# Performance work log

Hardware: AMD Instinct MI355X
Metric: run time of the kernel (lower is better)

The kernel has to match this reference:

```python
import jax, jax.numpy as jnp
import numpy as np

IMSIZE = 128; R = 2; B = 2; C = 3; D = 64; Q = 128; M = 8; ITERS = 32
N = IMSIZE * IMSIZE
EPS = 1e-8


def _build_edges(S, r):
    # local (2r+1)^2 pixel neighborhood, as in build_perception(imsize, perception_size)
    ys, xs = np.meshgrid(np.arange(S), np.arange(S), indexing='ij')
    rows, cols = [], []
    for dy in range(-r, r + 1):
        for dx in range(-r, r + 1):
            ny, nx = ys + dy, xs + dx
            ok = (ny >= 0) & (ny < S) & (nx >= 0) & (nx < S)
            rows.append((ys * S + xs)[ok])
            cols.append((ny * S + nx)[ok])
    return (np.concatenate(rows).astype(np.int32), np.concatenate(cols).astype(np.int32))


def _conv(x, w, b=None):
    y = jax.lax.conv_general_dilated(x, w, (1, 1), 'SAME', dimension_numbers=('NHWC', 'HWIO', 'NHWC'))
    return y if b is None else y + b


def _bn(x, g, b):
    mu = x.mean((0, 1, 2))
    var = x.var((0, 1, 2))
    return (x - mu) * jax.lax.rsqrt(var + 1e-5) * g + b


def _resblock(f, w1, g1, t1, w2, g2, t2):
    h = jax.nn.relu(_bn(_conv(f, w1), g1, t1))
    h = _bn(_conv(h, w2), g2, t2)
    return jax.nn.relu(f + h)


def _forward(x, w_bb1, b_bb1, w_bb2, b_bb2,
             w_k1, g_k1, t_k1, w_k2, g_k2, t_k2, w_kp, b_kp,
             w_q1, g_q1, t_q1, w_q2, g_q2, t_q2, w_qp,
             h0, row, col, agent_idx):
    # conv backbone (preserves spatial resolution)
    f = jax.nn.relu(_conv(x, w_bb1, b_bb1))
    f = jax.nn.relu(_conv(f, w_bb2, b_bb2))
    # key / query heads: ResidualBlock + 1x1 conv
    ks = _conv(_resblock(f, w_k1, g_k1, t_k1, w_k2, g_k2, t_k2), w_kp, b_kp).reshape(B, N, D)
    qs = _conv(_resblock(f, w_q1, g_q1, t_q1, w_q2, g_q2, t_q2), w_qp).reshape(B, N, D)
    # edge-gather cosine similarity (torch.cosine_similarity with eps=1e-8)
    qe = qs[:, row]          # [B, E, D]
    ke = ks[:, col]          # [B, E, D]
    weights = (qe * ke).sum(-1) / (
        jnp.maximum(jnp.linalg.norm(qe, axis=-1), EPS) *
        jnp.maximum(jnp.linalg.norm(ke, axis=-1), EPS))   # [B, E]

    # 32-iteration sparse adjacency propagation: h <- normalize(A @ h)
    def step(h, _):
        msg = jnp.zeros_like(h).at[:, row, :].add(weights[:, :, None] * h[:, col, :])
        h = msg / jnp.maximum(jnp.linalg.norm(msg, axis=-1, keepdims=True), EPS)
        return h, None

    h, _ = jax.lax.scan(step, h0, None, length=ITERS)     # [B, N, Q]

    # competition routing: pixels compete for M agent slots via cosine affinity
    pix = h / jnp.maximum(jnp.linalg.norm(h, axis=-1, keepdims=True), EPS)
    ag = pix[:, agent_idx]                                # [B, M, Q]
    sim = jnp.einsum('bnq,bmq->bnm', pix, ag)
    masks = jax.nn.softmax(sim * 10.0, axis=-1)           # [B, N, M]
    return masks.reshape(B, IMSIZE, IMSIZE, M).transpose(0, 3, 1, 2)  # [B, M, W, H]


def setup_inputs() -> dict:
    key = jax.random.key(0)
    k = jax.random.split(key, 12)
    s = 0.05
    row, col = _build_edges(IMSIZE, R)
    agent_idx = np.linspace(0, N - 1, M).astype(np.int32)
    return dict(
        x=jax.random.normal(k[0], (B, IMSIZE, IMSIZE, C), jnp.float32),
        w_bb1=jax.random.normal(k[1], (3, 3, C, D), jnp.float32) * s, b_bb1=jnp.zeros((D,), jnp.float32),
        w_bb2=jax.random.normal(k[2], (3, 3, D, D), jnp.float32) * s, b_bb2=jnp.zeros((D,), jnp.float32),
        w_k1=jax.random.normal(k[3], (3, 3, D, D), jnp.float32) * s,
        g_k1=jnp.ones((D,), jnp.float32), t_k1=jnp.zeros((D,), jnp.float32),
        w_k2=jax.random.normal(k[4], (3, 3, D, D), jnp.float32) * s,
        g_k2=jnp.ones((D,), jnp.float32), t_k2=jnp.zeros((D,), jnp.float32),
        w_kp=jax.random.normal(k[5], (1, 1, D, D), jnp.float32) * s, b_kp=jnp.zeros((D,), jnp.float32),
        w_q1=jax.random.normal(k[6], (3, 3, D, D), jnp.float32) * s,
        g_q1=jnp.ones((D,), jnp.float32), t_q1=jnp.zeros((D,), jnp.float32),
        w_q2=jax.random.normal(k[7], (3, 3, D, D), jnp.float32) * s,
        g_q2=jnp.ones((D,), jnp.float32), t_q2=jnp.zeros((D,), jnp.float32),
        w_qp=jax.random.normal(k[8], (1, 1, D, D), jnp.float32) * s,
        h0=jax.random.normal(k[9], (B, N, Q), jnp.float32),
        row=jnp.asarray(row), col=jnp.asarray(col),
        agent_idx=jnp.asarray(agent_idx),
    )


def reference(x, w_bb1, b_bb1, w_bb2, b_bb2,
              w_k1, g_k1, t_k1, w_k2, g_k2, t_k2, w_kp, b_kp,
              w_q1, g_q1, t_q1, w_q2, g_q2, t_q2, w_qp,
              h0, row, col, agent_idx):
    return _forward(x, w_bb1, b_bb1, w_bb2, b_bb2,
                    w_k1, g_k1, t_k1, w_k2, g_k2, t_k2, w_kp, b_kp,
                    w_q1, g_q1, t_q1, w_q2, g_q2, t_q2, w_qp,
                    h0, row, col, agent_idx)
```

## Files before the change

### kernel.cpp

```cpp
#include <hip/hip_runtime.h>
#include <math.h>

#define NPIX 16384
#define EPSF 1e-8f

typedef float f32x4 __attribute__((ext_vector_type(4)));
typedef short s16x8 __attribute__((ext_vector_type(8)));

__device__ __forceinline__ float wred64(float s){
  s += __shfl_xor(s, 32); s += __shfl_xor(s, 16); s += __shfl_xor(s, 8);
  s += __shfl_xor(s, 4);  s += __shfl_xor(s, 2);  s += __shfl_xor(s, 1);
  return s;
}
__device__ __forceinline__ float rdlane(float v, int l){
  return __int_as_float(__builtin_amdgcn_readlane(__float_as_int(v), l));
}
__device__ __forceinline__ float dot4f(float4 a, float4 b, float acc){
  acc = fmaf(a.x,b.x,acc); acc = fmaf(a.y,b.y,acc);
  acc = fmaf(a.z,b.z,acc); acc = fmaf(a.w,b.w,acc);
  return acc;
}
__device__ __forceinline__ void bf16split(float v, unsigned short &hi, unsigned short &lo){
  unsigned u = __float_as_uint(v);
  unsigned r = u + 0x7FFFu + ((u >> 16) & 1u);
  hi = (unsigned short)(r >> 16);
  float hf = __uint_as_float(((unsigned)hi) << 16);
  float l = v - hf;
  unsigned u2 = __float_as_uint(l);
  unsigned r2 = u2 + 0x7FFFu + ((u2 >> 16) & 1u);
  lo = (unsigned short)(r2 >> 16);
}

__global__ __launch_bounds__(256) void prep_kernel(const float* __restrict__ w_bb2, const float* __restrict__ w_k1,
                            const float* __restrict__ w_k2, const float* __restrict__ w_q1,
                            const float* __restrict__ w_q2, const float* __restrict__ w_kp,
                            const float* __restrict__ w_qp, unsigned short* __restrict__ wh,
                            unsigned short* __restrict__ wl, float* __restrict__ wtp,
                            float* __restrict__ stats){
  int gid = blockIdx.x*256 + threadIdx.x;
  if (gid < 184320){
    int j = gid & 7;
    int t1 = gid >> 3;
    int lane = t1 & 63;
    int t2 = t1 >> 6;
    int kb = t2 % 18;
    int t3 = t2 / 18;
    int ct = t3 & 3;
    int c  = t3 >> 2;
    const float* src = c==0? w_bb2 : c==1? w_k1 : c==2? w_k2 : c==3? w_q1 : w_q2;
    int cout = ct*16 + (lane & 15);
    int k = kb*32 + (lane>>4)*8 + j;
    float v = src[k*64 + cout];
    unsigned short h,l; bf16split(v,h,l);
    wh[gid] = h; wl[gid] = l;
  } else if (gid < 192512){
    int t = gid - 184320; int which = t >> 12; int d = t & 4095;
    const float* src = which ? w_qp : w_kp;
    int k = d & 3, cout = (d>>2) & 63, cin4 = d >> 8;
    wtp[t] = src[(cin4*4 + k)*64 + cout];
  } else if (gid < 193024){
    stats[gid - 192512] = 0.f;
  }
}

__global__ __launch_bounds__(256) void conv1_kernel(const float* __restrict__ x, const float* __restrict__ w,
                                                    const float* __restrict__ bias, float* __restrict__ out){
  int wv = blockIdx.x*4 + (threadIdx.x >> 6);
  int c  = threadIdx.x & 63;
  int p0 = wv << 3;
  int ub = __builtin_amdgcn_readfirstlane(p0);
  int b  = ub >> 14; int i0 = ub & (NPIX-1);
  int y  = i0 >> 7, x0 = i0 & 127;
  float wv_[9][3];
  #pragma unroll
  for (int t=0;t<9;++t)
    #pragma unroll
    for (int ci=0;ci<3;++ci) wv_[t][ci] = w[(t*3+ci)*64 + c];
  float bv = bias[c];
  float acc[8];
  #pragma unroll
  for (int p=0;p<8;++p) acc[p] = bv;
  for (int ky=0; ky<3; ++ky){
    int ny = y + ky - 1;
    if ((unsigned)ny >= 128u) continue;
    const float* rowp = x + ((b<<14) + ny*128)*3;
    for (int kx=0; kx<3; ++kx){
      int t = ky*3 + kx;
      #pragma unroll
      for (int p=0;p<8;++p){
        int col = x0 + p + kx - 1;
        if ((unsigned)col < 128u){
          const float* ip = rowp + col*3;
          acc[p] = fmaf(ip[0], wv_[t][0], acc[p]);
          acc[p] = fmaf(ip[1], wv_[t][1], acc[p]);
          acc[p] = fmaf(ip[2], wv_[t][2], acc[p]);
        }
      }
    }
  }
  float* op = out + (p0 << 6) + c;
  #pragma unroll
  for (int p=0;p<8;++p) op[p*64] = fmaxf(acc[p], 0.f);
}

__global__ __launch_bounds__(512) void conv3m_kernel(const float* __restrict__ in,
    const unsigned short* __restrict__ wh, const unsigned short* __restrict__ wl,
    const float* __restrict__ bias, int relu,
    const float* __restrict__ bnst, const float* __restrict__ bng, const float* __restrict__ bnb,
    float* __restrict__ out, float* __restrict__ ost){
  __shared__ unsigned short lhi[12672];
  __shared__ unsigned short llo[12672];
  __shared__ float lout[4352];
  __shared__ float la[64], lb[64];
  __shared__ float ls1[64], ls2[64];
  int blk = blockIdx.x;
  int xh = blk & 1, y = (blk>>1) & 127, b = blk >> 8;
  int x0 = xh << 6;
  int tid = threadIdx.x;
  if (tid < 64){
    float a = 1.f, bo = 0.f;
    if (bnst){
      float mu  = bnst[tid] * (1.f/32768.f);
      float var = bnst[64+tid] * (1.f/32768.f) - mu*mu;
      a  = bng[tid] * rsqrtf(var + 1e-5f);
      bo = bnb[tid] - mu*a;
    }
    la[tid] = a; lb[tid] = bo;
    ls1[tid] = 0.f; ls2[tid] = 0.f;
  }
  __syncthreads();
  for (int s = tid; s < 3168; s += 512){
    int pr = s >> 4, cq = s & 15;
    int ky = pr / 66, px = pr - ky*66;
    int ny = y + ky - 1, gx = x0 - 1 + px;
    float v0=0.f, v1=0.f, v2=0.f, v3=0.f;
    if ((unsigned)ny < 128u && (unsigned)gx < 128u){
      const float* ip = in + (((b<<14) + ny*128 + gx)<<6) + (cq<<2);
      float4 t = *(const float4*)ip;
      int c0 = cq<<2;
      v0 = fmaxf(fmaf(t.x, la[c0],   lb[c0]),   0.f);
      v1 = fmaxf(fmaf(t.y, la[c0+1], lb[c0+1]), 0.f);
      v2 = fmaxf(fmaf(t.z, la[c0+2], lb[c0+2]), 0.f);
      v3 = fmaxf(fmaf(t.w, la[c0+3], lb[c0+3]), 0.f);
    }
    unsigned short h0,l0,h1,l1,h2,l2,h3,l3;
    bf16split(v0,h0,l0); bf16split(v1,h1,l1); bf16split(v2,h2,l2); bf16split(v3,h3,l3);
    int slot = (cq >> 1) ^ (pr & 7);
    int byte = pr*128 + (slot<<4) + ((cq & 1) << 3);
    *(uint2*)((char*)lhi + byte) = make_uint2((unsigned)h0 | ((unsigned)h1<<16),
                                              (unsigned)h2 | ((unsigned)h3<<16));
    *(uint2*)((char*)llo + byte) = make_uint2((unsigned)l0 | ((unsigned)l1<<16),
                                              (unsigned)l2 | ((unsigned)l3<<16));
  }
  __syncthreads();
  int lane = tid & 63, wid = tid >> 6;
  int pxsub = wid & 3, ch = wid >> 2;
  int col16 = lane & 15, kgrp = lane >> 4;
  f32x4 acc0 = {0.f,0.f,0.f,0.f}, acc1 = acc0, acl0 = acc0, acl1 = acc0;
  int abase = (ch*2*18)*512 + lane*8;
  #pragma unroll
  for (int kb=0; kb<18; ++kb){
    int tap = kb >> 1;
    int ky = (tap >= 6) ? 2 : (tap >= 3 ? 1 : 0);
    int kx = tap - ky*3;
    int pr = ky*66 + pxsub*16 + col16 + kx;
    int ci0 = ((kb & 1) << 5) + (kgrp << 3);
    int byte = pr*128 + ((((ci0 >> 3) ^ (pr & 7))) << 4);
    s16x8 Bh = *(const s16x8*)((const char*)lhi + byte);
    s16x8 Bl = *(const s16x8*)((const char*)llo + byte);
    int ao = abase + kb*512;
    s16x8 Ah0 = *(const s16x8*)(wh + ao);
    s16x8 Al0 = *(const s16x8*)(wl + ao);
    s16x8 Ah1 = *(const s16x8*)(wh + ao + 9216);
    s16x8 Al1 = *(const s16x8*)(wl + ao + 9216);
    acc0 = __builtin_amdgcn_mfma_f32_16x16x32_bf16(Ah0, Bh, acc0, 0, 0, 0);
    acl0 = __builtin_amdgcn_mfma_f32_16x16x32_bf16(Ah0, Bl, acl0, 0, 0, 0);
    acc1 = __builtin_amdgcn_mfma_f32_16x16x32_bf16(Ah1, Bh, acc1, 0, 0, 0);
    acl1 = __builtin_amdgcn_mfma_f32_16x16x32_bf16(Ah1, Bl, acl1, 0, 0, 0);
    acl0 = __builtin_amdgcn_mfma_f32_16x16x32_bf16(Al0, Bh, acl0, 0, 0, 0);
    acl1 = __builtin_amdgcn_mfma_f32_16x16x32_bf16(Al1, Bh, acl1, 0, 0, 0);
  }
  acc0 = acc0 + acl0;
  acc1 = acc1 + acl1;
  int pxl = pxsub*16 + col16;
  int co0 = ch*32 + kgrp*4;
  *(f32x4*)(lout + pxl*68 + co0)      = acc0;
  *(f32x4*)(lout + pxl*68 + co0 + 16) = acc1;
  __syncthreads();
  {
    int px = tid >> 3, c8 = (tid & 7) << 3;
    const float* lp = lout + px*68 + c8;
    float r0[8];
    #pragma unroll
    for (int j=0;j<8;++j) r0[j] = lp[j];
    if (bias){
      #pragma unroll
      for (int j=0;j<8;++j) r0[j] += bias[c8+j];
    }
    if (relu){
      #pragma unroll
      for (int j=0;j<8;++j) r0[j] = fmaxf(r0[j], 0.f);
    }
    float* op = out + (((b<<14) + y*128 + x0 + px)<<6) + c8;
    #pragma unroll
    for (int j=0;j<8;++j) op[j] = r0[j];
    if (ost){
      float s1v[8], s2v[8];
      #pragma unroll
      for (int j=0;j<8;++j){ s1v[j] = r0[j]; s2v[j] = r0[j]*r0[j]; }
      #pragma unroll
      for (int m=8; m<64; m<<=1){
        #pragma unroll
        for (int j=0;j<8;++j){ s1v[j] += __shfl_xor(s1v[j], m); s2v[j] += __shfl_xor(s2v[j], m); }
      }
      int lane2 = tid & 63;
      if ((lane2 >> 3) == 0){
        int c0 = (lane2 & 7) << 3;
        #pragma unroll
        for (int j=0;j<8;++j){ atomicAdd(&ls1[c0+j], s1v[j]); atomicAdd(&ls2[c0+j], s2v[j]); }
      }
      __syncthreads();
      if (tid < 64){ atomicAdd(&ost[tid], ls1[tid]); atomicAdd(&ost[64+tid], ls2[tid]); }
    }
  }
}

__global__ __launch_bounds__(256) void resfuse_kernel(float* __restrict__ t, const float* __restrict__ f,
                                                      const float* __restrict__ stats, const float* __restrict__ g,
                                                      const float* __restrict__ beta){
  int idx4 = blockIdx.x*256 + threadIdx.x;
  float4 v = ((float4*)t)[idx4];
  float4 fv = ((const float4*)f)[idx4];
  int c0 = (idx4 & 15) * 4;
  float a[4], bb[4];
  #pragma unroll
  for (int j=0;j<4;++j){
    int c = c0 + j;
    float mu  = stats[c]    * (1.f/32768.f);
    float var = stats[64+c] * (1.f/32768.f) - mu*mu;
    a[j]  = g[c] * rsqrtf(var + 1e-5f);
    bb[j] = beta[c] - mu*a[j];
  }
  v.x = fmaxf(fv.x + fmaf(v.x, a[0], bb[0]), 0.f);
  v.y = fmaxf(fv.y + fmaf(v.y, a[1], bb[1]), 0.f);
  v.z = fmaxf(fv.z + fmaf(v.z, a[2], bb[2]), 0.f);
  v.w = fmaxf(fv.w + fmaf(v.w, a[3], bb[3]), 0.f);
  ((float4*)t)[idx4] = v;
}

__global__ __launch_bounds__(256) void proj_kernel(const float* __restrict__ r, const float* __restrict__ wt1,
                                                   const float* __restrict__ bias, float* __restrict__ out,
                                                   float* __restrict__ nrm){
  int wv = blockIdx.x*4 + (threadIdx.x >> 6);
  int c  = threadIdx.x & 63;
  int p0 = wv << 3;
  int ub = __builtin_amdgcn_readfirstlane(p0);
  const float4* wq = (const float4*)wt1 + c;
  float4 w[16];
  #pragma unroll
  for (int q=0;q<16;++q) w[q] = wq[q*64];
  float bv = bias ? bias[c] : 0.f;
  #pragma unroll
  for (int p=0;p<8;++p){
    const float* ip = r + ((ub + p) << 6);
    float a0 = bv, a1 = 0.f;
    #pragma unroll
    for (int q=0;q<16;q+=2){
      float4 i0 = *(const float4*)(ip + (q<<2));
      float4 i1 = *(const float4*)(ip + ((q+1)<<2));
      a0 = dot4f(i0, w[q],   a0);
      a1 = dot4f(i1, w[q+1], a1);
    }
    float acc = a0 + a1;
    out[((p0+p)<<6) + c] = acc;
    float s = wred64(acc*acc);
    if (c == 0) nrm[p0+p] = sqrtf(s);
  }
}

#define EW_PAD 68
__global__ __launch_bounds__(256) void edge_kernel(const float* __restrict__ qs, const float* __restrict__ ks,
                                                   const float* __restrict__ nq, const float* __restrict__ nk,
                                                   float* __restrict__ W){
  __shared__ float klds[100*EW_PAD];
  __shared__ float qlds[16*EW_PAD];
  int blk = blockIdx.x;
  int b = blk >> 10; int rem = blk & 1023;
  int y = rem >> 3; int x0 = (rem & 7) << 4;
  int tid = threadIdx.x;
  for (int s = tid; s < 1600; s += 256){
    int cin4 = s & 15; int col = (s >> 4) % 20; int r = (s >> 4) / 20;
    int ry = y - 2 + r; ry = ry < 0 ? 0 : (ry > 127 ? 127 : ry);
    int cx = x0 - 2 + col; cx = cx < 0 ? 0 : (cx > 127 ? 127 : cx);
    float4 v = *(const float4*)(ks + (((b<<14) + ry*128 + cx)<<6) + cin4*4);
    *(float4*)(klds + (r*20+col)*EW_PAD + cin4*4) = v;
  }
  {
    int cin4 = tid & 15; int px = tid >> 4;
    float4 v = *(const float4*)(qs + (((b<<14) + y*128 + x0 + px)<<6) + cin4*4);
    *(float4*)(qlds + px*EW_PAD + cin4*4) = v;
  }
  __syncthreads();
  #pragma unroll
  for (int pair=0; pair<2; ++pair){
    int t2 = tid + pair*256;
    int px = t2 >> 5; int o = t2 & 31;
    if (o < 25){
      int dy = o/5 - 2, dx = o%5 - 2;
      int yy = y + dy, xx = x0 + px + dx;
      bool valid = ((unsigned)yy < 128u) && ((unsigned)xx < 128u);
      const float* kq = klds + ((dy+2)*20 + (px+dx+2))*EW_PAD;
      const float* qq = qlds + px*EW_PAD;
      float a0 = 0.f, a1 = 0.f;
      #pragma unroll
      for (int q=0; q<16; q+=2){
        a0 = dot4f(*(const float4*)(qq + q*4),     *(const float4*)(kq + q*4),     a0);
        a1 = dot4f(*(const float4*)(qq + (q+1)*4), *(const float4*)(kq + (q+1)*4), a1);
      }
      float acc = a0 + a1;
      int gp = (b<<14) + y*128 + x0 + px;
      float wv_ = 0.f;
      if (valid){
        int gj = (b<<14) + yy*128 + xx;
        float rq = 1.f / fmaxf(nq[gp], EPSF);
        float rk = 1.f / fmaxf(nk[gj], EPSF);
        wv_ = acc * rq * rk;
      }
      W[gp*25 + o] = wv_;
    }
  }
}

__global__ __launch_bounds__(256) void mp_iter_kernel(const float* __restrict__ src, float* __restrict__ dst,
                                                      const float* __restrict__ W){
  int lane = threadIdx.x & 63;
  int wid  = threadIdx.x >> 6;
  int blk  = blockIdx.x;
  int xcd = blk & 7, s = blk >> 3;
  int row_id = xcd*32 + (s >> 2);
  int q4 = s & 3;
  int b = row_id >> 7, y = row_id & 127;
  int x0 = ((q4 << 2) + wid) << 3;
  int gp0 = (b << 14) + y*128 + x0;
  int lo = lane < 25 ? lane : 24;
  float wv[8];
  #pragma unroll
  for (int p=0;p<8;++p) wv[p] = W[(gp0+p)*25 + lo];
  const float* rp[5];
  #pragma unroll
  for (int r=0;r<5;++r){
    int ry = y - 2 + r; ry = ry < 0 ? 0 : (ry > 127 ? 127 : ry);
    rp[r] = src + (((b<<14) + ry*128) << 7) + lane;
  }
  float wa[5][5], wb[5][5];
  #pragma unroll
  for (int cc=0; cc<4; ++cc){
    int xc = x0 - 2 + cc; if (xc < 0) xc = 0;
    int off = xc << 7;
    #pragma unroll
    for (int r=0;r<5;++r){ wa[r][cc] = rp[r][off]; wb[r][cc] = rp[r][off + 64]; }
  }
  #pragma unroll
  for (int p=0;p<8;++p){
    int xl = x0 + p + 2; if (xl > 127) xl = 127;
    int off = xl << 7;
    #pragma unroll
    for (int r=0;r<5;++r){ wa[r][4] = rp[r][off]; wb[r][4] = rp[r][off + 64]; }
    float a0 = 0.f, a1 = 0.f;
    #pragma unroll
    for (int r=0;r<5;++r){
      #pragma unroll
      for (int cc=0;cc<5;++cc){
        float w = rdlane(wv[p], r*5+cc);
        a0 = fmaf(w, wa[r][cc], a0);
        a1 = fmaf(w, wb[r][cc], a1);
      }
    }
    float ss = wred64(a0*a0 + a1*a1);
    float sc = 1.f / fmaxf(sqrtf(ss), EPSF);
    float* dp = dst + ((gp0 + p) << 7) + lane;
    dp[0] = a0*sc; dp[64] = a1*sc;
    #pragma unroll
    for (int r=0;r<5;++r){
      #pragma unroll
      for (int cc=0;cc<4;++cc){ wa[r][cc] = wa[r][cc+1]; wb[r][cc] = wb[r][cc+1]; }
    }
  }
}

__global__ void mp_agents_kernel(const float* __restrict__ hf, const int* __restrict__ agidx,
                                 float* __restrict__ agbuf){
  int lane = threadIdx.x & 63; int w = threadIdx.x >> 6;
  int ab = w >> 3, m = w & 7;
  int ai = agidx[m];
  const float* hp = hf + (((ab<<14) + ai) << 7) + lane;
  float v0 = hp[0], v1 = hp[64];
  float ss = wred64(v0*v0 + v1*v1);
  float sc = 1.f / fmaxf(sqrtf(ss), EPSF);
  float* ap = agbuf + (((ab<<3) + m) << 7) + lane;
  ap[0] = v0*sc; ap[64] = v1*sc;
}

__global__ __launch_bounds__(256) void mp_final_kernel(const float* __restrict__ hf, const float* __restrict__ agbuf,
                                                       float* __restrict__ out){
  int lane = threadIdx.x & 63;
  int wid  = threadIdx.x >> 6;
  int blk  = blockIdx.x;
  int xcd = blk & 7, s = blk >> 3;
  int row_id = xcd*32 + (s >> 2);
  int q4 = s & 3;
  int b = row_id >> 7, y = row_id & 127;
  int x0 = ((q4 << 2) + wid) << 3;
  int gp0 = (b << 14) + y*128 + x0;
  #pragma unroll 1
  for (int p=0;p<8;++p){
    int gp = gp0 + p;
    const float* hp = hf + (gp << 7) + lane;
    float v0 = hp[0], v1 = hp[64];
    float ss = wred64(v0*v0 + v1*v1);
    float sc = 1.f / fmaxf(sqrtf(ss), EPSF);
    float p0 = v0*sc, p1 = v1*sc;
    float sim[8];
    #pragma unroll
    for (int m=0;m<8;++m){
      const float* ap = agbuf + (((b<<3) + m) << 7) + lane;
      sim[m] = wred64(p0*ap[0] + p1*ap[64]);
    }
    float mx = sim[0];
    #pragma unroll
    for (int m=1;m<8;++m) mx = fmaxf(mx, sim[m]);
    float e[8]; float sum = 0.f;
    #pragma unroll
    for (int m=0;m<8;++m){ e[m] = __expf((sim[m]-mx)*10.f); sum += e[m]; }
    float rs = 1.f / sum;
    if (lane < 8){
      float val = e[0];
      #pragma unroll
      for (int m=1;m<8;++m) val = (lane==m) ? e[m] : val;
      out[(((b<<3)+lane)<<14) + y*128 + x0 + p] = val * rs;
    }
  }
}

extern "C" void kernel_launch(void* const* d_in, const int* in_sizes, int n_in,
                              void* d_out, int out_size, void* d_ws, size_t ws_size,
                              hipStream_t stream) {
  (void)in_sizes; (void)n_in; (void)out_size; (void)ws_size;
  const float* x     = (const float*)d_in[0];
  const float* w_bb1 = (const float*)d_in[1];
  const float* b_bb1 = (const float*)d_in[2];
  const float* w_bb2 = (const float*)d_in[3];
  const float* b_bb2 = (const float*)d_in[4];
  const float* w_k1  = (const float*)d_in[5];
  const float* g_k1  = (const float*)d_in[6];
  const float* t_k1  = (const float*)d_in[7];
  const float* w_k2  = (const float*)d_in[8];
  const float* g_k2  = (const float*)d_in[9];
  const float* t_k2  = (const float*)d_in[10];
  const float* w_kp  = (const float*)d_in[11];
  const float* b_kp  = (const float*)d_in[12];
  const float* w_q1  = (const float*)d_in[13];
  const float* g_q1  = (const float*)d_in[14];
  const float* t_q1  = (const float*)d_in[15];
  const float* w_q2  = (const float*)d_in[16];
  const float* g_q2  = (const float*)d_in[17];
  const float* t_q2  = (const float*)d_in[18];
  const float* w_qp  = (const float*)d_in[19];
  const float* h0    = (const float*)d_in[20];
  const int*   agidx = (const int*)d_in[23];
  float* out = (float*)d_out;
  float* ws  = (float*)d_ws;

  float* S0 = ws + 0;
  float* S1 = ws + 2097152;
  float* S2 = ws + 4194304;
  float* S3 = ws + 6291456;
  float* S4 = ws + 8388608;
  float* WW = ws + 12582912;
  float* NK = ws + 13402112;
  float* NQ = ws + 13434880;
  float* ST = ws + 13467648;
  float* AG = ws + 13468160;
  float* WTp = ws + 13470208;
  unsigned short* WH = (unsigned short*)(ws + 13478400);
  unsigned short* WL = WH + 184320;
  float* HA = ws + 0;
  float* HB = ws + 4194304;

  prep_kernel<<<754, 256, 0, stream>>>(w_bb2, w_k1, w_k2, w_q1, w_q2, w_kp, w_qp, WH, WL, WTp, ST);
  conv1_kernel<<<1024, 256, 0, stream>>>(x, w_bb1, b_bb1, S0);
  conv3m_kernel<<<512, 512, 0, stream>>>(S0, WH + 0, WL + 0, b_bb2, 1, nullptr, nullptr, nullptr, S1, nullptr);
  conv3m_kernel<<<512, 512, 0, stream>>>(S1, WH + 36864, WL + 36864, nullptr, 0, nullptr, nullptr, nullptr, S2, ST + 0);
  conv3m_kernel<<<512, 512, 0, stream>>>(S1, WH + 3*36864, WL + 3*36864, nullptr, 0, nullptr, nullptr, nullptr, S3, ST + 256);
  conv3m_kernel<<<512, 512, 0, stream>>>(S2, WH + 2*36864, WL + 2*36864, nullptr, 0, ST + 0, g_k1, t_k1, S0, ST + 128);
  resfuse_kernel<<<2048, 256, 0, stream>>>(S0, S1, ST + 128, g_k2, t_k2);
  proj_kernel<<<1024, 256, 0, stream>>>(S0, WTp + 0, b_kp, S4, NK);
  conv3m_kernel<<<512, 512, 0, stream>>>(S3, WH + 4*36864, WL + 4*36864, nullptr, 0, ST + 256, g_q1, t_q1, S2, ST + 384);
  resfuse_kernel<<<2048, 256, 0, stream>>>(S2, S1, ST + 384, g_q2, t_q2);
  proj_kernel<<<1024, 256, 0, stream>>>(S2, WTp + 4096, nullptr, S3, NQ);
  edge_kernel<<<2048, 256, 0, stream>>>(S3, S4, NQ, NK, WW);
  const float* sbuf = h0;
  for (int it = 0; it < 32; ++it){
    float* dbuf = (it & 1) ? HB : HA;
    mp_iter_kernel<<<1024, 256, 0, stream>>>(sbuf, dbuf, WW);
    sbuf = dbuf;
  }
  mp_agents_kernel<<<1, 1024, 0, stream>>>(HB, agidx, AG);
  mp_final_kernel<<<1024, 256, 0, stream>>>(HB, AG, out);
}
```

Before: 637.2 us.

## Fuse paired first residual convs, halve per-wave MP work, fold agent normalization

Adds a conv3m2 kernel that computes the key and query first residual convolutions from the same shared-memory input tile, so the staging and bf16 split of S1 happen once instead of twice. The 32 message-passing iteration launches now use twice as many blocks, each wave handling 4 pixels instead of 8, to raise parallelism at the cost of more redundant halo loads. The separate agents-normalization kernel is removed and its work is folded into mp_final, saving one launch while every block recomputes the 8 agent norms.

```diff
diff --git a/kernel.cpp b/kernel.cpp
--- a/kernel.cpp
+++ b/kernel.cpp
@@ -225,6 +225,124 @@
   }
 }
 
+__global__ __launch_bounds__(512) void conv3m2_kernel(const float* __restrict__ in,
+    const unsigned short* __restrict__ whA, const unsigned short* __restrict__ wlA,
+    const unsigned short* __restrict__ whB, const unsigned short* __restrict__ wlB,
+    float* __restrict__ outA, float* __restrict__ ostA,
+    float* __restrict__ outB, float* __restrict__ ostB){
+  __shared__ unsigned short lhi[12672];
+  __shared__ unsigned short llo[12672];
+  __shared__ float lout[4352];
+  __shared__ float ls1A[64], ls2A[64], ls1B[64], ls2B[64];
+  int blk = blockIdx.x;
+  int xh = blk & 1, y = (blk>>1) & 127, b = blk >> 8;
+  int x0 = xh << 6;
+  int tid = threadIdx.x;
+  if (tid < 64){ ls1A[tid]=0.f; ls2A[tid]=0.f; ls1B[tid]=0.f; ls2B[tid]=0.f; }
+  __syncthreads();
+  for (int s = tid; s < 3168; s += 512){
+    int pr = s >> 4, cq = s & 15;
+    int ky = pr / 66, px = pr - ky*66;
+    int ny = y + ky - 1, gx = x0 - 1 + px;
+    float v0=0.f, v1=0.f, v2=0.f, v3=0.f;
+    if ((unsigned)ny < 128u && (unsigned)gx < 128u){
+      const float* ip = in + (((b<<14) + ny*128 + gx)<<6) + (cq<<2);
+      float4 t = *(const float4*)ip;
+      v0 = t.x; v1 = t.y; v2 = t.z; v3 = t.w;
+    }
+    unsigned short h0,l0,h1,l1,h2,l2,h3,l3;
+    bf16split(v0,h0,l0); bf16split(v1,h1,l1); bf16split(v2,h2,l2); bf16split(v3,h3,l3);
+    int slot = (cq >> 1) ^ (pr & 7);
+    int byte = pr*128 + (slot<<4) + ((cq & 1) << 3);
+    *(uint2*)((char*)lhi + byte) = make_uint2((unsigned)h0 | ((unsigned)h1<<16),
+                                              (unsigned)h2 | ((unsigned)h3<<16));
+    *(uint2*)((char*)llo + byte) = make_uint2((unsigned)l0 | ((unsigned)l1<<16),
+                                              (unsigned)l2 | ((unsigned)l3<<16));
+  }
+  __syncthreads();
+  int lane = tid & 63, wid = tid >> 6;
+  int pxsub = wid & 3, ch = wid >> 2;
+  int col16 = lane & 15, kgrp = lane >> 4;
+  f32x4 z = {0.f,0.f,0.f,0.f};
+  f32x4 aA0=z, aA1=z, lA0=z, lA1=z, aB0=z, aB1=z, lB0=z, lB1=z;
+  int abase = (ch*2*18)*512 + lane*8;
+  #pragma unroll
+  for (int kb=0; kb<18; ++kb){
+    int tap = kb >> 1;
+    int ky = (tap >= 6) ? 2 : (tap >= 3 ? 1 : 0);
+    int kx = tap - ky*3;
+    int pr = ky*66 + pxsub*16 + col16 + kx;
+    int ci0 = ((kb & 1) << 5) + (kgrp << 3);
+    int byte = pr*128 + ((((ci0 >> 3) ^ (pr & 7))) << 4);
+    s16x8 Bh = *(const s16x8*)((const char*)lhi + byte);
+    s16x8 Bl = *(const s16x8*)((const char*)llo + byte);
+    int ao = abase + kb*512;
+    s16x8 AhA0 = *(const s16x8*)(whA + ao);
+    s16x8 AlA0 = *(const s16x8*)(wlA + ao);
+    s16x8 AhA1 = *(const s16x8*)(whA + ao + 9216);
+    s16x8 AlA1 = *(const s16x8*)(wlA + ao + 9216);
+    s16x8 AhB0 = *(const s16x8*)(whB + ao);
+    s16x8 AlB0 = *(const s16x8*)(wlB + ao);
+    s16x8 AhB1 = *(const s16x8*)(whB + ao + 9216);
+    s16x8 AlB1 = *(const s16x8*)(wlB + ao + 9216);
+    aA0 = __builtin_amdgcn_mfma_f32_16x16x32_bf16(AhA0, Bh, aA0, 0, 0, 0);
+    lA0 = __builtin_amdgcn_mfma_f32_16x16x32_bf16(AhA0, Bl, lA0, 0, 0, 0);
+    aA1 = __builtin_amdgcn_mfma_f32_16x16x32_bf16(AhA1, Bh, aA1, 0, 0, 0);
+    lA1 = __builtin_amdgcn_mfma_f32_16x16x32_bf16(AhA1, Bl, lA1, 0, 0, 0);
+    lA0 = __builtin_amdgcn_mfma_f32_16x16x32_bf16(AlA0, Bh, lA0, 0, 0, 0);
+    lA1 = __builtin_amdgcn_mfma_f32_16x16x32_bf16(AlA1, Bh, lA1, 0, 0, 0);
+    aB0 = __builtin_amdgcn_mfma_f32_16x16x32_bf16(AhB0, Bh, aB0, 0, 0, 0);
+    lB0 = __builtin_amdgcn_mfma_f32_16x16x32_bf16(AhB0, Bl, lB0, 0, 0, 0);
+    aB1 = __builtin_amdgcn_mfma_f32_16x16x32_bf16(AhB1, Bh, aB1, 0, 0, 0);
+    lB1 = __builtin_amdgcn_mfma_f32_16x16x32_bf16(AhB1, Bl, lB1, 0, 0, 0);
+    lB0 = __builtin_amdgcn_mfma_f32_16x16x32_bf16(AlB0, Bh, lB0, 0, 0, 0);
+    lB1 = __builtin_amdgcn_mfma_f32_16x16x32_bf16(AlB1, Bh, lB1, 0, 0, 0);
+  }
+  aA0 = aA0 + lA0; aA1 = aA1 + lA1;
+  aB0 = aB0 + lB0; aB1 = aB1 + lB1;
+  int pxl = pxsub*16 + col16;
+  int co0 = ch*32 + kgrp*4;
+  int px = tid >> 3, c8 = (tid & 7) << 3;
+  int lane2 = tid & 63;
+  #pragma unroll
+  for (int phase=0; phase<2; ++phase){
+    f32x4 w0 = phase ? aB0 : aA0;
+    f32x4 w1 = phase ? aB1 : aA1;
+    float* outp = phase ? outB : outA;
+    float* ostp = phase ? ostB : ostA;
+    float* lsp1 = phase ? ls1B : ls1A;
+    float* lsp2 = phase ? ls2B : ls2A;
+    *(f32x4*)(lout + pxl*68 + co0)      = w0;
+    *(f32x4*)(lout + pxl*68 + co0 + 16) = w1;
+    __syncthreads();
+    const float* lp = lout + px*68 + c8;
+    float r0[8];
+    #pragma unroll
+    for (int j=0;j<8;++j) r0[j] = lp[j];
+    float* op = outp + (((b<<14) + y*128 + x0 + px)<<6) + c8;
+    #pragma unroll
+    for (int j=0;j<8;++j) op[j] = r0[j];
+    float s1v[8], s2v[8];
+    #pragma unroll
+    for (int j=0;j<8;++j){ s1v[j] = r0[j]; s2v[j] = r0[j]*r0[j]; }
+    #pragma unroll
+    for (int m=8; m<64; m<<=1){
+      #pragma unroll
+      for (int j=0;j<8;++j){ s1v[j] += __shfl_xor(s1v[j], m); s2v[j] += __shfl_xor(s2v[j], m); }
+    }
+    if ((lane2 >> 3) == 0){
+      int c0 = (lane2 & 7) << 3;
+      #pragma unroll
+      for (int j=0;j<8;++j){ atomicAdd(&lsp1[c0+j], s1v[j]); atomicAdd(&lsp2[c0+j], s2v[j]); }
+    }
+    __syncthreads();
+  }
+  if (tid < 64){
+    atomicAdd(&ostA[tid], ls1A[tid]); atomicAdd(&ostA[64+tid], ls2A[tid]);
+    atomicAdd(&ostB[tid], ls1B[tid]); atomicAdd(&ostB[64+tid], ls2B[tid]);
+  }
+}
+
 __global__ __launch_bounds__(256) void resfuse_kernel(float* __restrict__ t, const float* __restrict__ f,
                                                       const float* __restrict__ stats, const float* __restrict__ g,
                                                       const float* __restrict__ beta){
@@ -337,15 +455,15 @@
   int wid  = threadIdx.x >> 6;
   int blk  = blockIdx.x;
   int xcd = blk & 7, s = blk >> 3;
-  int row_id = xcd*32 + (s >> 2);
-  int q4 = s & 3;
+  int row_id = xcd*32 + (s >> 3);
+  int q8 = s & 7;
   int b = row_id >> 7, y = row_id & 127;
-  int x0 = ((q4 << 2) + wid) << 3;
+  int x0 = ((q8 << 2) + wid) << 2;
   int gp0 = (b << 14) + y*128 + x0;
   int lo = lane < 25 ? lane : 24;
-  float wv[8];
-  #pragma unroll
-  for (int p=0;p<8;++p) wv[p] = W[(gp0+p)*25 + lo];
+  float wv[4];
+  #pragma unroll
+  for (int p=0;p<4;++p) wv[p] = W[(gp0+p)*25 + lo];
   const float* rp[5];
   #pragma unroll
   for (int r=0;r<5;++r){
@@ -361,7 +479,7 @@
     for (int r=0;r<5;++r){ wa[r][cc] = rp[r][off]; wb[r][cc] = rp[r][off + 64]; }
   }
   #pragma unroll
-  for (int p=0;p<8;++p){
+  for (int p=0;p<4;++p){
     int xl = x0 + p + 2; if (xl > 127) xl = 127;
     int off = xl << 7;
     #pragma unroll
@@ -388,20 +506,7 @@
   }
 }
 
-__global__ void mp_agents_kernel(const float* __restrict__ hf, const int* __restrict__ agidx,
-                                 float* __restrict__ agbuf){
-  int lane = threadIdx.x & 63; int w = threadIdx.x >> 6;
-  int ab = w >> 3, m = w & 7;
-  int ai = agidx[m];
-  const float* hp = hf + (((ab<<14) + ai) << 7) + lane;
-  float v0 = hp[0], v1 = hp[64];
-  float ss = wred64(v0*v0 + v1*v1);
-  float sc = 1.f / fmaxf(sqrtf(ss), EPSF);
-  float* ap = agbuf + (((ab<<3) + m) << 7) + lane;
-  ap[0] = v0*sc; ap[64] = v1*sc;
-}
-
-__global__ __launch_bounds__(256) void mp_final_kernel(const float* __restrict__ hf, const float* __restrict__ agbuf,
+__global__ __launch_bounds__(256) void mp_final_kernel(const float* __restrict__ hf, const int* __restrict__ agidx,
                                                        float* __restrict__ out){
   int lane = threadIdx.x & 63;
   int wid  = threadIdx.x >> 6;
@@ -412,6 +517,15 @@
   int b = row_id >> 7, y = row_id & 127;
   int x0 = ((q4 << 2) + wid) << 3;
   int gp0 = (b << 14) + y*128 + x0;
+  float av0[8], av1[8], isc[8];
+  #pragma unroll
+  for (int m=0;m<8;++m){
+    int ai = agidx[m];
+    const float* ap = hf + (((b<<14) + ai) << 7) + lane;
+    av0[m] = ap[0]; av1[m] = ap[64];
+    float ssm = wred64(av0[m]*av0[m] + av1[m]*av1[m]);
+    isc[m] = 1.f / fmaxf(sqrtf(ssm), EPSF);
+  }
   #pragma unroll 1
   for (int p=0;p<8;++p){
     int gp = gp0 + p;
@@ -422,10 +536,8 @@
     float p0 = v0*sc, p1 = v1*sc;
     float sim[8];
     #pragma unroll
-    for (int m=0;m<8;++m){
-      const float* ap = agbuf + (((b<<3) + m) << 7) + lane;
-      sim[m] = wred64(p0*ap[0] + p1*ap[64]);
-    }
+    for (int m=0;m<8;++m)
+      sim[m] = wred64(p0*av0[m] + p1*av1[m]) * isc[m];
     float mx = sim[0];
     #pragma unroll
     for (int m=1;m<8;++m) mx = fmaxf(mx, sim[m]);
@@ -480,7 +592,6 @@
   float* NK = ws + 13402112;
   float* NQ = ws + 13434880;
   float* ST = ws + 13467648;
-  float* AG = ws + 13468160;
   float* WTp = ws + 13470208;
   unsigned short* WH = (unsigned short*)(ws + 13478400);
   unsigned short* WL = WH + 184320;
@@ -490,8 +601,8 @@
   prep_kernel<<<754, 256, 0, stream>>>(w_bb2, w_k1, w_k2, w_q1, w_q2, w_kp, w_qp, WH, WL, WTp, ST);
   conv1_kernel<<<1024, 256, 0, stream>>>(x, w_bb1, b_bb1, S0);
   conv3m_kernel<<<512, 512, 0, stream>>>(S0, WH + 0, WL + 0, b_bb2, 1, nullptr, nullptr, nullptr, S1, nullptr);
-  conv3m_kernel<<<512, 512, 0, stream>>>(S1, WH + 36864, WL + 36864, nullptr, 0, nullptr, nullptr, nullptr, S2, ST + 0);
-  conv3m_kernel<<<512, 512, 0, stream>>>(S1, WH + 3*36864, WL + 3*36864, nullptr, 0, nullptr, nullptr, nullptr, S3, ST + 256);
+  conv3m2_kernel<<<512, 512, 0, stream>>>(S1, WH + 36864, WL + 36864, WH + 3*36864, WL + 3*36864,
+                                          S2, ST + 0, S3, ST + 256);
   conv3m_kernel<<<512, 512, 0, stream>>>(S2, WH + 2*36864, WL + 2*36864, nullptr, 0, ST + 0, g_k1, t_k1, S0, ST + 128);
   resfuse_kernel<<<2048, 256, 0, stream>>>(S0, S1, ST + 128, g_k2, t_k2);
   proj_kernel<<<1024, 256, 0, stream>>>(S0, WTp + 0, b_kp, S4, NK);
@@ -502,9 +613,8 @@
   const float* sbuf = h0;
   for (int it = 0; it < 32; ++it){
     float* dbuf = (it & 1) ? HB : HA;
-    mp_iter_kernel<<<1024, 256, 0, stream>>>(sbuf, dbuf, WW);
+    mp_iter_kernel<<<2048, 256, 0, stream>>>(sbuf, dbuf, WW);
     sbuf = dbuf;
   }
-  mp_agents_kernel<<<1, 1024, 0, stream>>>(HB, agidx, AG);
-  mp_final_kernel<<<1024, 256, 0, stream>>>(HB, AG, out);
-}
+  mp_final_kernel<<<1024, 256, 0, stream>>>(HB, agidx, out);
+}
```

Measured after the change: 605.5 us. 5.0% less time.
